# Optimization experiments

Hardware: AMD Instinct MI355X
Metric: run time of the kernel (lower is better)

Reference implementation:

```python
import jax, jax.numpy as jnp
import numpy as np

NUM_TAGS = 256
BATCH = 64
SEQ = 512


def setup_inputs() -> dict:
    key = jax.random.key(0)
    k1, k2, k3 = jax.random.split(key, 3)
    logits = jax.random.normal(k1, (BATCH, SEQ, NUM_TAGS), dtype=jnp.float32)
    tags = jax.random.randint(k2, (BATCH, SEQ), 0, NUM_TAGS, dtype=jnp.int32)
    mask = jnp.ones((BATCH, SEQ), dtype=jnp.int32)
    # learned parameter: transitions [K, K] (xavier-normal-ish init)
    std = float(np.sqrt(2.0 / (NUM_TAGS + NUM_TAGS)))
    transitions = jax.random.normal(k3, (NUM_TAGS, NUM_TAGS), dtype=jnp.float32) * std
    return {"logits": logits, "tags": tags, "mask": mask, "transitions": transitions}


def _input_likelihood(logits, mask, transitions):
    # logits: [B, S, K], mask: [B, S] float
    logits_t = jnp.transpose(logits, (1, 0, 2))  # [S, B, K]
    mask_t = jnp.transpose(mask, (1, 0))         # [S, B]
    alpha0 = logits_t[0]                          # [B, K]

    def step(alpha, xs):
        logit_i, mask_i = xs                      # [B, K], [B]
        # inner: [B, K_prev, K_next]
        inner = alpha[:, :, None] + logit_i[:, None, :] + transitions[None, :, :]
        new_alpha = jax.nn.logsumexp(inner, axis=1)
        m = mask_i[:, None]
        alpha = new_alpha * m + alpha * (1.0 - m)
        return alpha, None

    alpha, _ = jax.lax.scan(step, alpha0, (logits_t[1:], mask_t[1:]))
    return jax.nn.logsumexp(alpha, axis=-1)      # [B]


def _joint_likelihood(logits, tags, mask, transitions):
    # logits: [B, S, K], tags: [B, S] int, mask: [B, S] float
    B, S, K = logits.shape
    # transition scores for steps 0..S-2 -> transitions[tags[i], tags[i+1]] * mask[i+1]
    trans = transitions[tags[:, :-1], tags[:, 1:]] * mask[:, 1:]      # [B, S-1]
    # emit scores for steps 0..S-2 -> logits[i, tags[i]] * mask[i]
    emit = jnp.take_along_axis(logits[:, :-1], tags[:, :-1, None], axis=-1)[..., 0] * mask[:, :-1]
    score = trans.sum(axis=1) + emit.sum(axis=1)                      # [B]
    # last valid tag per batch (mask is a contiguous prefix)
    last_idx = mask.sum(axis=1).astype(jnp.int32) - 1                 # [B]
    last_tags = jnp.take_along_axis(tags, last_idx[:, None], axis=1)[:, 0]
    last_input = logits[:, -1, :][jnp.arange(B), last_tags]           # [B]
    score = score + last_input * mask[:, -1]
    return score


def reference(logits, tags, mask, transitions):
    mask_f = mask.astype(logits.dtype)
    log_num = _joint_likelihood(logits, tags, mask_f, transitions)
    log_den = _input_likelihood(logits, mask_f, transitions)
    return jnp.sum(log_num - log_den)
```

## Files before the change

### kernel.cpp

```cpp
#include <hip/hip_runtime.h>
#include <stdint.h>

#define NTAGS 256
#define BATCH 64
#define SEQ   512
#define MB    16
#define NTHREADS 256

typedef __attribute__((ext_vector_type(8))) short short8;
typedef __attribute__((ext_vector_type(4))) float f32x4;

__device__ __forceinline__ unsigned int f32_to_bf16_bits(float f) {
  unsigned int u = __float_as_uint(f);
  return (u + 0x7FFFu + ((u >> 16) & 1u)) >> 16;
}
__device__ __forceinline__ float wave_sum(float v) {
#pragma unroll
  for (int o = 32; o; o >>= 1) v += __shfl_xor(v, o);
  return v;
}
__device__ __forceinline__ unsigned int pk_bf16(float lo, float hi) {
  unsigned int r;
  asm("v_cvt_pk_bf16_f32 %0, %1, %2" : "=v"(r) : "v"(lo), "v"(hi));
  return r;
}

#define LOG2E 1.4426950408889634f

#define BAR_LGKM() \
    asm volatile("s_waitcnt lgkmcnt(0)" ::: "memory"); \
    __builtin_amdgcn_s_barrier(); \
    asm volatile("" ::: "memory");

#define MFMA_ALL(RB) \
    f32x4 acc0 = {0.f,0.f,0.f,0.f}, acc1 = {0.f,0.f,0.f,0.f}, \
          acc2 = {0.f,0.f,0.f,0.f}, acc3 = {0.f,0.f,0.f,0.f}; \
    _Pragma("unroll") \
    for (int c = 0; c < 8; ++c) { \
      const short8 bf = *(const short8*)&alds[RB][bidxs[c]]; \
      acc0 = __builtin_amdgcn_mfma_f32_16x16x32_bf16(aF[0][c], bf, acc0, 0, 0, 0); \
      acc1 = __builtin_amdgcn_mfma_f32_16x16x32_bf16(aF[1][c], bf, acc1, 0, 0, 0); \
      acc2 = __builtin_amdgcn_mfma_f32_16x16x32_bf16(aF[2][c], bf, acc2, 0, 0, 0); \
      acc3 = __builtin_amdgcn_mfma_f32_16x16x32_bf16(aF[3][c], bf, acc3, 0, 0, 0); \
    }

#define EPI_TILE_F(I, ACCI, PB, WB) { \
      const uint2 pw = PB[I]; \
      const float p0 = __uint_as_float(pw.x << 16); \
      const float p1 = __uint_as_float(pw.x & 0xFFFF0000u); \
      const float p2 = __uint_as_float(pw.y << 16); \
      const float p3 = __uint_as_float(pw.y & 0xFFFF0000u); \
      const float n0 = (MM ? ACCI[0] * p0 : sOld[I][0]) * sc; \
      const float n1 = (MM ? ACCI[1] * p1 : sOld[I][1]) * sc; \
      const float n2 = (MM ? ACCI[2] * p2 : sOld[I][2]) * sc; \
      const float n3 = (MM ? ACCI[3] * p3 : sOld[I][3]) * sc; \
      sOld[I][0] = n0; sOld[I][1] = n1; sOld[I][2] = n2; sOld[I][3] = n3; \
      mxl = fmaxf(mxl, fmaxf(fmaxf(n0, n1), fmaxf(n2, n3))); \
      uint2 wv; wv.x = pk_bf16(n0, n1); wv.y = pk_bf16(n2, n3); \
      *(uint2*)&alds[WB][widx[I]] = wv; }

#define EPI_TILE_B(I, ACCI, PB, WB) { \
      const uint2 pw = PB[I]; \
      const float p0 = __uint_as_float(pw.x << 16); \
      const float p1 = __uint_as_float(pw.x & 0xFFFF0000u); \
      const float p2 = __uint_as_float(pw.y << 16); \
      const float p3 = __uint_as_float(pw.y & 0xFFFF0000u); \
      float n0, n1, n2, n3; \
      if (fastm) { \
        n0 = ACCI[0] * p0 * sc; n1 = ACCI[1] * p1 * sc; \
        n2 = ACCI[2] * p2 * sc; n3 = ACCI[3] * p3 * sc; \
      } else { \
        const float q0 = __uint_as_float(gp[I].x << 16); \
        const float q1 = __uint_as_float(gp[I].x & 0xFFFF0000u); \
        const float q2 = __uint_as_float(gp[I].y << 16); \
        const float q3 = __uint_as_float(gp[I].y & 0xFFFF0000u); \
        n0 = (MM ? ACCI[0] * p0 : sOld[I][0] * (p0 / q0)) * sc; \
        n1 = (MM ? ACCI[1] * p1 : sOld[I][1] * (p1 / q1)) * sc; \
        n2 = (MM ? ACCI[2] * p2 : sOld[I][2] * (p2 / q2)) * sc; \
        n3 = (MM ? ACCI[3] * p3 : sOld[I][3] * (p3 / q3)) * sc; \
      } \
      gp[I] = pw; \
      sOld[I][0] = n0; sOld[I][1] = n1; sOld[I][2] = n2; sOld[I][3] = n3; \
      mxl = fmaxf(mxl, fmaxf(fmaxf(n0, n1), fmaxf(n2, n3))); \
      uint2 wv; wv.x = pk_bf16(n0, n1); wv.y = pk_bf16(n2, n3); \
      *(uint2*)&alds[WB][widx[I]] = wv; }

#define STEPF(T, RB, WB, PC, PL, MC, ML, APPLY, MEAS) { \
    { const int tp_ = ((T) + 2 < SEQ) ? ((T) + 2) : (SEQ - 1); \
      _Pragma("unroll") \
      for (int i2 = 0; i2 < 4; ++i2) PL[i2] = *(const uint2*)(Pp + tp_ * NTAGS + 16 * i2); \
      ML = mkp[tp_]; } \
    MFMA_ALL(RB) \
    float sc = 1.0f; \
    if (APPLY) { \
      const f32x4 mx4 = *(const f32x4*)&maxw[p][0]; \
      const float mx = fmaxf(fmaxf(mx4[0], mx4[1]), fmaxf(mx4[2], mx4[3])); \
      const int e = (int)((__float_as_uint(mx) >> 23) & 0xFF) - 127; \
      esum += e; \
      sc = __uint_as_float((unsigned int)(127 - e) << 23); \
    } \
    const int MM = MC; \
    float mxl = -3.0e38f; \
    EPI_TILE_F(0, acc0, PC, WB) EPI_TILE_F(1, acc1, PC, WB) \
    EPI_TILE_F(2, acc2, PC, WB) EPI_TILE_F(3, acc3, PC, WB) \
    if (MEAS) { \
      float v = mxl; v = fmaxf(v, __shfl_xor(v, 16)); v = fmaxf(v, __shfl_xor(v, 32)); \
      if (q == 0) maxw[p][wid] = v; \
    } \
    BAR_LGKM() }

#define STEPB(T, RB, WB, PC, PL, MC, ML, APPLY, MEAS) { \
    { const int tp_ = ((T) >= 2) ? ((T) - 2) : 0; \
      const int tm_ = ((T) >= 1) ? ((T) - 1) : 0; \
      _Pragma("unroll") \
      for (int i2 = 0; i2 < 4; ++i2) PL[i2] = *(const uint2*)(Pp + tp_ * NTAGS + 16 * i2); \
      ML = mkp[tm_]; } \
    MFMA_ALL(RB) \
    float sc = 1.0f; \
    if (APPLY) { \
      const f32x4 mx4 = *(const f32x4*)&maxw[p][0]; \
      const float mx = fmaxf(fmaxf(mx4[0], mx4[1]), fmaxf(mx4[2], mx4[3])); \
      const int e = (int)((__float_as_uint(mx) >> 23) & 0xFF) - 127; \
      esum += e; \
      sc = __uint_as_float((unsigned int)(127 - e) << 23); \
    } \
    const int MM = MC; \
    const bool fastm = (bool)__all(MM != 0); \
    float mxl = -3.0e38f; \
    EPI_TILE_B(0, acc0, PC, WB) EPI_TILE_B(1, acc1, PC, WB) \
    EPI_TILE_B(2, acc2, PC, WB) EPI_TILE_B(3, acc3, PC, WB) \
    if (MEAS) { \
      float v = mxl; v = fmaxf(v, __shfl_xor(v, 16)); v = fmaxf(v, __shfl_xor(v, 32)); \
      if (q == 0) maxw[p][wid] = v; \
    } \
    BAR_LGKM() }

__global__ __launch_bounds__(256)
void crf_prep(const float* __restrict__ lg, unsigned int* __restrict__ P)
{
  const size_t g = (size_t)blockIdx.x * 256 + threadIdx.x;
  const float4 a = ((const float4*)lg)[2 * g];
  const float4 b = ((const float4*)lg)[2 * g + 1];
  uint4 o;
  o.x = pk_bf16(exp2f(a.x * LOG2E), exp2f(a.y * LOG2E));
  o.y = pk_bf16(exp2f(a.z * LOG2E), exp2f(a.w * LOG2E));
  o.z = pk_bf16(exp2f(b.x * LOG2E), exp2f(b.y * LOG2E));
  o.w = pk_bf16(exp2f(b.z * LOG2E), exp2f(b.w * LOG2E));
  ((uint4*)P)[g] = o;
}

__global__ __launch_bounds__(NTHREADS, 1)
void crf_halves(const unsigned short* __restrict__ P,
                const int*   __restrict__ mask,
                const float* __restrict__ trans,
                float* __restrict__ wsA, float* __restrict__ wsB,
                int* __restrict__ wseF, int* __restrict__ wseB)
{
  const int bid  = blockIdx.x;
  const int bwd  = bid >> 2;
  const int b0   = (bid & 3) * MB;
  const int tid  = threadIdx.x;
  const int wid  = tid >> 6;
  const int lane = tid & 63;
  const int p    = lane & 15;
  const int q    = lane >> 4;

  __shared__ __align__(16) short alds[2][NTAGS * MB];
  __shared__ __align__(16) float maxw[16][4];

  const unsigned short* Pp = P + (size_t)(b0 + p) * SEQ * NTAGS + 64 * wid + 4 * q;
  const int* mkp = mask + (b0 + p) * SEQ;

  int bidxs[8], widx[4];
#pragma unroll
  for (int c = 0; c < 8; ++c) bidxs[c] = (p * NTAGS + 32 * c + 8 * q) ^ ((p & 7) << 3);
#pragma unroll
  for (int i = 0; i < 4; ++i) widx[i] = (p * NTAGS + 64 * wid + 16 * i + 4 * q) ^ ((p & 7) << 3);

  short8 aF[4][8];
#pragma unroll
  for (int i = 0; i < 4; ++i) {
    const int m = 64 * wid + 16 * i + p;
#pragma unroll
    for (int c = 0; c < 8; ++c) {
      short8 w;
#pragma unroll
      for (int j = 0; j < 8; ++j) {
        const int tag = 32 * c + 8 * q + j;
        const float tv = bwd ? trans[m * NTAGS + tag] : trans[tag * NTAGS + m];
        w[j] = (short)f32_to_bf16_bits(exp2f(tv * LOG2E));
      }
      aF[i][c] = w;
    }
  }

  f32x4 sOld[4];
  uint2 p0[4], p1[4], p2[4], p3[4], gp[4];
  int m0 = 1, m1 = 1, m2 = 1, m3 = 1;
  int esum = 0;

  if (!bwd) {
#pragma unroll
    for (int i = 0; i < 4; ++i) {
      const uint2 pw = *(const uint2*)(Pp + 16 * i);
      f32x4 a;
      a[0] = __uint_as_float(pw.x << 16); a[1] = __uint_as_float(pw.x & 0xFFFF0000u);
      a[2] = __uint_as_float(pw.y << 16); a[3] = __uint_as_float(pw.y & 0xFFFF0000u);
      sOld[i] = a;
      *(uint2*)&alds[0][widx[i]] = pw;
    }
#pragma unroll
    for (int i = 0; i < 4; ++i) {
      p1[i] = *(const uint2*)(Pp + 1 * NTAGS + 16 * i);
      p2[i] = *(const uint2*)(Pp + 2 * NTAGS + 16 * i);
    }
    m1 = mkp[1]; m2 = mkp[2];
    __syncthreads();

    STEPF(1, 0, 1, p1, p3, m1, m3, 0, 0)
    STEPF(2, 1, 0, p2, p0, m2, m0, 0, 0)
    STEPF(3, 0, 1, p3, p1, m3, m1, 0, 1)
#pragma unroll 1
    for (int tb = 4; tb <= 248; tb += 4) {
      STEPF(tb + 0, 1, 0, p0, p2, m0, m2, 1, 0)
      STEPF(tb + 1, 0, 1, p1, p3, m1, m3, 0, 0)
      STEPF(tb + 2, 1, 0, p2, p0, m2, m0, 0, 0)
      STEPF(tb + 3, 0, 1, p3, p1, m3, m1, 0, 1)
    }
    STEPF(252, 1, 0, p0, p2, m0, m2, 1, 0)
    STEPF(253, 0, 1, p1, p3, m1, m3, 0, 0)
    STEPF(254, 1, 0, p2, p0, m2, m0, 0, 0)

    {
      MFMA_ALL(0)
      const int MM = m3;
      float* wp = wsA + (size_t)(b0 + p) * NTAGS + 64 * wid + 4 * q;
#pragma unroll
      for (int i = 0; i < 4; ++i) {
        const uint2 pw = p3[i];
        f32x4 pv;
        pv[0] = __uint_as_float(pw.x << 16); pv[1] = __uint_as_float(pw.x & 0xFFFF0000u);
        pv[2] = __uint_as_float(pw.y << 16); pv[3] = __uint_as_float(pw.y & 0xFFFF0000u);
        f32x4 o;
        const f32x4 ac = (i == 0) ? acc0 : (i == 1) ? acc1 : (i == 2) ? acc2 : acc3;
#pragma unroll
        for (int r = 0; r < 4; ++r)
          o[r] = MM ? ac[r] * pv[r] : sOld[i][r];
        *(f32x4*)(wp + 16 * i) = o;
      }
    }
    if (tid < 16) wseF[b0 + tid] = esum;
  } else {
#pragma unroll
    for (int i = 0; i < 4; ++i) {
      const uint2 pw = *(const uint2*)(Pp + (SEQ - 1) * NTAGS + 16 * i);
      f32x4 a;
      a[0] = __uint_as_float(pw.x << 16); a[1] = __uint_as_float(pw.x & 0xFFFF0000u);
      a[2] = __uint_as_float(pw.y << 16); a[3] = __uint_as_float(pw.y & 0xFFFF0000u);
      sOld[i] = a; gp[i] = pw;
      *(uint2*)&alds[0][widx[i]] = pw;
    }
#pragma unroll
    for (int i = 0; i < 4; ++i) {
      p2[i] = *(const uint2*)(Pp + 510 * NTAGS + 16 * i);
      p1[i] = *(const uint2*)(Pp + 509 * NTAGS + 16 * i);
    }
    m2 = mkp[511];
    m1 = mkp[510];
    __syncthreads();

    STEPB(510, 0, 1, p2, p0, m2, m0, 0, 0)
    STEPB(509, 1, 0, p1, p3, m1, m3, 0, 0)
    STEPB(508, 0, 1, p0, p2, m0, m2, 0, 1)
#pragma unroll 1
    for (int tb = 507; tb >= 263; tb -= 4) {
      STEPB(tb - 0, 1, 0, p3, p1, m3, m1, 1, 0)
      STEPB(tb - 1, 0, 1, p2, p0, m2, m0, 0, 0)
      STEPB(tb - 2, 1, 0, p1, p3, m1, m3, 0, 0)
      STEPB(tb - 3, 0, 1, p0, p2, m0, m2, 0, 1)
    }
    STEPB(259, 1, 0, p3, p1, m3, m1, 1, 0)
    STEPB(258, 0, 1, p2, p0, m2, m0, 0, 0)
    STEPB(257, 1, 0, p1, p3, m1, m3, 0, 0)
    STEPB(256, 0, 1, p0, p2, m0, m2, 0, 0)

    {
      MFMA_ALL(1)
      float* wp = wsB + (size_t)(b0 + p) * NTAGS + 64 * wid + 4 * q;
      *(f32x4*)(wp + 0)  = acc0;
      *(f32x4*)(wp + 16) = acc1;
      *(f32x4*)(wp + 32) = acc2;
      *(f32x4*)(wp + 48) = acc3;
    }
    if (tid < 16) wseB[b0 + tid] = esum;
  }
}

__global__ __launch_bounds__(256)
void crf_combine(const float* __restrict__ logits,
                 const int*   __restrict__ tags,
                 const int*   __restrict__ mask,
                 const float* __restrict__ trans,
                 const float* __restrict__ wsA,
                 const float* __restrict__ wsB,
                 const int*   __restrict__ wseF,
                 const int*   __restrict__ wseB,
                 float* __restrict__ out)
{
  const int b    = blockIdx.x;
  const int tid  = threadIdx.x;
  const int lane = tid & 63;
  const int wid  = tid >> 6;

  __shared__ float rn[4], rm[4], rp[4];

  const float LN2 = 0.6931471805599453f;
  const float* lg = logits + (size_t)b * SEQ * NTAGS;
  const int*   tg = tags + b * SEQ;
  const int*   mk = mask + b * SEQ;

  float numer = 0.f, msum = 0.f;
  for (int t = tid; t < SEQ; t += 256) {
    int   tag_t = tg[t];
    float m_t   = (float)mk[t];
    msum += m_t;
    if (t < SEQ - 1) {
      numer += lg[t * NTAGS + tag_t] * m_t;
      numer += trans[tag_t * NTAGS + tg[t + 1]] * (float)mk[t + 1];
    }
  }
  numer = wave_sum(numer);
  msum  = wave_sum(msum);
  if (lane == 0) { rn[wid] = numer; rm[wid] = msum; }

  float pprod = wsA[b * NTAGS + tid] * wsB[b * NTAGS + tid];
  pprod = wave_sum(pprod);
  if (lane == 0) rp[wid] = pprod;
  __syncthreads();

  if (tid == 0) {
    const float numer_tot = (rn[0] + rn[1]) + (rn[2] + rn[3]);
    const float msum_tot  = (rm[0] + rm[1]) + (rm[2] + rm[3]);
    const float psum      = (rp[0] + rp[1]) + (rp[2] + rp[3]);
    const float log_den   = logf(psum) + (float)(wseF[b] + wseB[b]) * LN2;
    int last_idx = (int)msum_tot - 1;
    if (last_idx < 0) last_idx = 0;
    const int last_tag = tg[last_idx];
    const float score = numer_tot + lg[(SEQ - 1) * NTAGS + last_tag] * (float)mk[SEQ - 1];
    atomicAdd(out, score - log_den);
  }
}

extern "C" void kernel_launch(void* const* d_in, const int* in_sizes, int n_in,
                              void* d_out, int out_size, void* d_ws, size_t ws_size,
                              hipStream_t stream) {
  const float* logits = (const float*)d_in[0];
  const int*   tags   = (const int*)d_in[1];
  const int*   mask   = (const int*)d_in[2];
  const float* trans  = (const float*)d_in[3];
  float* out = (float*)d_out;

  unsigned short* P = (unsigned short*)d_ws;
  float* wsA  = (float*)((char*)d_ws + (size_t)BATCH * SEQ * NTAGS * 2);
  float* wsB  = wsA + BATCH * NTAGS;
  int*   wseF = (int*)(wsB + BATCH * NTAGS);
  int*   wseB = wseF + BATCH;

  hipMemsetAsync(out, 0, sizeof(float), stream);
  crf_prep<<<dim3(BATCH * SEQ * NTAGS / (256 * 8)), dim3(256), 0, stream>>>(logits, (unsigned int*)P);
  crf_halves<<<dim3(8), dim3(NTHREADS), 0, stream>>>(P, mask, trans, wsA, wsB, wseF, wseB);
  crf_combine<<<dim3(BATCH), dim3(256), 0, stream>>>(logits, tags, mask, trans, wsA, wsB, wseF, wseB, out);
}
```

Baseline: 286.0 us.

## Merge forward and backward chains into one 512-thread block per batch group

```diff
diff --git a/kernel.cpp b/kernel.cpp
--- a/kernel.cpp
+++ b/kernel.cpp
@@ -5,7 +5,7 @@
 #define BATCH 64
 #define SEQ   512
 #define MB    16
-#define NTHREADS 256
+#define NTHREADS 512
 
 typedef __attribute__((ext_vector_type(8))) short short8;
 typedef __attribute__((ext_vector_type(4))) float f32x4;
@@ -37,88 +37,56 @@
           acc2 = {0.f,0.f,0.f,0.f}, acc3 = {0.f,0.f,0.f,0.f}; \
     _Pragma("unroll") \
     for (int c = 0; c < 8; ++c) { \
-      const short8 bf = *(const short8*)&alds[RB][bidxs[c]]; \
+      const short8 bf = *(const short8*)&aldsC[RB][bidxs[c]]; \
       acc0 = __builtin_amdgcn_mfma_f32_16x16x32_bf16(aF[0][c], bf, acc0, 0, 0, 0); \
       acc1 = __builtin_amdgcn_mfma_f32_16x16x32_bf16(aF[1][c], bf, acc1, 0, 0, 0); \
       acc2 = __builtin_amdgcn_mfma_f32_16x16x32_bf16(aF[2][c], bf, acc2, 0, 0, 0); \
       acc3 = __builtin_amdgcn_mfma_f32_16x16x32_bf16(aF[3][c], bf, acc3, 0, 0, 0); \
     }
 
-#define EPI_TILE_F(I, ACCI, PB, WB) { \
+#define EPI_TILE(I, ACCI, PB, WB, ME) { \
       const uint2 pw = PB[I]; \
-      const float p0 = __uint_as_float(pw.x << 16); \
-      const float p1 = __uint_as_float(pw.x & 0xFFFF0000u); \
-      const float p2 = __uint_as_float(pw.y << 16); \
-      const float p3 = __uint_as_float(pw.y & 0xFFFF0000u); \
-      const float n0 = (MM ? ACCI[0] * p0 : sOld[I][0]) * sc; \
-      const float n1 = (MM ? ACCI[1] * p1 : sOld[I][1]) * sc; \
-      const float n2 = (MM ? ACCI[2] * p2 : sOld[I][2]) * sc; \
-      const float n3 = (MM ? ACCI[3] * p3 : sOld[I][3]) * sc; \
-      sOld[I][0] = n0; sOld[I][1] = n1; sOld[I][2] = n2; sOld[I][3] = n3; \
-      mxl = fmaxf(mxl, fmaxf(fmaxf(n0, n1), fmaxf(n2, n3))); \
-      uint2 wv; wv.x = pk_bf16(n0, n1); wv.y = pk_bf16(n2, n3); \
-      *(uint2*)&alds[WB][widx[I]] = wv; }
-
-#define EPI_TILE_B(I, ACCI, PB, WB) { \
-      const uint2 pw = PB[I]; \
-      const float p0 = __uint_as_float(pw.x << 16); \
-      const float p1 = __uint_as_float(pw.x & 0xFFFF0000u); \
-      const float p2 = __uint_as_float(pw.y << 16); \
-      const float p3 = __uint_as_float(pw.y & 0xFFFF0000u); \
+      const float p0_ = __uint_as_float(pw.x << 16); \
+      const float p1_ = __uint_as_float(pw.x & 0xFFFF0000u); \
+      const float p2_ = __uint_as_float(pw.y << 16); \
+      const float p3_ = __uint_as_float(pw.y & 0xFFFF0000u); \
       float n0, n1, n2, n3; \
       if (fastm) { \
-        n0 = ACCI[0] * p0 * sc; n1 = ACCI[1] * p1 * sc; \
-        n2 = ACCI[2] * p2 * sc; n3 = ACCI[3] * p3 * sc; \
+        n0 = ACCI[0] * p0_ * sc; n1 = ACCI[1] * p1_ * sc; \
+        n2 = ACCI[2] * p2_ * sc; n3 = ACCI[3] * p3_ * sc; \
+      } else if (!chain) { \
+        n0 = (MM ? ACCI[0] * p0_ : sOld[I][0]) * sc; \
+        n1 = (MM ? ACCI[1] * p1_ : sOld[I][1]) * sc; \
+        n2 = (MM ? ACCI[2] * p2_ : sOld[I][2]) * sc; \
+        n3 = (MM ? ACCI[3] * p3_ : sOld[I][3]) * sc; \
       } else { \
-        const float q0 = __uint_as_float(gp[I].x << 16); \
-        const float q1 = __uint_as_float(gp[I].x & 0xFFFF0000u); \
-        const float q2 = __uint_as_float(gp[I].y << 16); \
-        const float q3 = __uint_as_float(gp[I].y & 0xFFFF0000u); \
-        n0 = (MM ? ACCI[0] * p0 : sOld[I][0] * (p0 / q0)) * sc; \
-        n1 = (MM ? ACCI[1] * p1 : sOld[I][1] * (p1 / q1)) * sc; \
-        n2 = (MM ? ACCI[2] * p2 : sOld[I][2] * (p2 / q2)) * sc; \
-        n3 = (MM ? ACCI[3] * p3 : sOld[I][3] * (p3 / q3)) * sc; \
+        const float q0_ = __uint_as_float(gp[I].x << 16); \
+        const float q1_ = __uint_as_float(gp[I].x & 0xFFFF0000u); \
+        const float q2_ = __uint_as_float(gp[I].y << 16); \
+        const float q3_ = __uint_as_float(gp[I].y & 0xFFFF0000u); \
+        n0 = (MM ? ACCI[0] * p0_ : sOld[I][0] * (p0_ / q0_)) * sc; \
+        n1 = (MM ? ACCI[1] * p1_ : sOld[I][1] * (p1_ / q1_)) * sc; \
+        n2 = (MM ? ACCI[2] * p2_ : sOld[I][2] * (p2_ / q2_)) * sc; \
+        n3 = (MM ? ACCI[3] * p3_ : sOld[I][3] * (p3_ / q3_)) * sc; \
       } \
       gp[I] = pw; \
       sOld[I][0] = n0; sOld[I][1] = n1; sOld[I][2] = n2; sOld[I][3] = n3; \
-      mxl = fmaxf(mxl, fmaxf(fmaxf(n0, n1), fmaxf(n2, n3))); \
+      if (ME) mxl = fmaxf(mxl, fmaxf(fmaxf(n0, n1), fmaxf(n2, n3))); \
       uint2 wv; wv.x = pk_bf16(n0, n1); wv.y = pk_bf16(n2, n3); \
-      *(uint2*)&alds[WB][widx[I]] = wv; }
-
-#define STEPF(T, RB, WB, PC, PL, MC, ML, APPLY, MEAS) { \
-    { const int tp_ = ((T) + 2 < SEQ) ? ((T) + 2) : (SEQ - 1); \
+      *(uint2*)&aldsC[WB][widx[I]] = wv; }
+
+#define STEP(S, RB, WB, PC, PL, MC, ML, APPLY, MEAS) { \
+    { int tpP_ = chain ? 509 - (S) : (S) + 2; \
+      int tpM_ = chain ? 510 - (S) : (S) + 2; \
+      tpP_ = tpP_ < 0 ? 0 : (tpP_ > SEQ - 1 ? SEQ - 1 : tpP_); \
+      tpM_ = tpM_ < 0 ? 0 : (tpM_ > SEQ - 1 ? SEQ - 1 : tpM_); \
       _Pragma("unroll") \
-      for (int i2 = 0; i2 < 4; ++i2) PL[i2] = *(const uint2*)(Pp + tp_ * NTAGS + 16 * i2); \
-      ML = mkp[tp_]; } \
+      for (int i2 = 0; i2 < 4; ++i2) PL[i2] = *(const uint2*)(Pp + (size_t)tpP_ * NTAGS + 16 * i2); \
+      ML = mkp[tpM_]; } \
     MFMA_ALL(RB) \
     float sc = 1.0f; \
     if (APPLY) { \
-      const f32x4 mx4 = *(const f32x4*)&maxw[p][0]; \
-      const float mx = fmaxf(fmaxf(mx4[0], mx4[1]), fmaxf(mx4[2], mx4[3])); \
-      const int e = (int)((__float_as_uint(mx) >> 23) & 0xFF) - 127; \
-      esum += e; \
-      sc = __uint_as_float((unsigned int)(127 - e) << 23); \
-    } \
-    const int MM = MC; \
-    float mxl = -3.0e38f; \
-    EPI_TILE_F(0, acc0, PC, WB) EPI_TILE_F(1, acc1, PC, WB) \
-    EPI_TILE_F(2, acc2, PC, WB) EPI_TILE_F(3, acc3, PC, WB) \
-    if (MEAS) { \
-      float v = mxl; v = fmaxf(v, __shfl_xor(v, 16)); v = fmaxf(v, __shfl_xor(v, 32)); \
-      if (q == 0) maxw[p][wid] = v; \
-    } \
-    BAR_LGKM() }
-
-#define STEPB(T, RB, WB, PC, PL, MC, ML, APPLY, MEAS) { \
-    { const int tp_ = ((T) >= 2) ? ((T) - 2) : 0; \
-      const int tm_ = ((T) >= 1) ? ((T) - 1) : 0; \
-      _Pragma("unroll") \
-      for (int i2 = 0; i2 < 4; ++i2) PL[i2] = *(const uint2*)(Pp + tp_ * NTAGS + 16 * i2); \
-      ML = mkp[tm_]; } \
-    MFMA_ALL(RB) \
-    float sc = 1.0f; \
-    if (APPLY) { \
-      const f32x4 mx4 = *(const f32x4*)&maxw[p][0]; \
+      const f32x4 mx4 = *(const f32x4*)&maxwC[p][0]; \
       const float mx = fmaxf(fmaxf(mx4[0], mx4[1]), fmaxf(mx4[2], mx4[3])); \
       const int e = (int)((__float_as_uint(mx) >> 23) & 0xFF) - 127; \
       esum += e; \
@@ -127,11 +95,11 @@
     const int MM = MC; \
     const bool fastm = (bool)__all(MM != 0); \
     float mxl = -3.0e38f; \
-    EPI_TILE_B(0, acc0, PC, WB) EPI_TILE_B(1, acc1, PC, WB) \
-    EPI_TILE_B(2, acc2, PC, WB) EPI_TILE_B(3, acc3, PC, WB) \
+    EPI_TILE(0, acc0, PC, WB, MEAS) EPI_TILE(1, acc1, PC, WB, MEAS) \
+    EPI_TILE(2, acc2, PC, WB, MEAS) EPI_TILE(3, acc3, PC, WB, MEAS) \
     if (MEAS) { \
       float v = mxl; v = fmaxf(v, __shfl_xor(v, 16)); v = fmaxf(v, __shfl_xor(v, 32)); \
-      if (q == 0) maxw[p][wid] = v; \
+      if (q == 0) maxwC[p][cw] = v; \
     } \
     BAR_LGKM() }
 
@@ -156,38 +124,42 @@
                 float* __restrict__ wsA, float* __restrict__ wsB,
                 int* __restrict__ wseF, int* __restrict__ wseB)
 {
-  const int bid  = blockIdx.x;
-  const int bwd  = bid >> 2;
-  const int b0   = (bid & 3) * MB;
-  const int tid  = threadIdx.x;
-  const int wid  = tid >> 6;
-  const int lane = tid & 63;
-  const int p    = lane & 15;
-  const int q    = lane >> 4;
-
-  __shared__ __align__(16) short alds[2][NTAGS * MB];
-  __shared__ __align__(16) float maxw[16][4];
-
-  const unsigned short* Pp = P + (size_t)(b0 + p) * SEQ * NTAGS + 64 * wid + 4 * q;
+  const int bid   = blockIdx.x;
+  const int b0    = bid * MB;
+  const int tid   = threadIdx.x;
+  const int wid   = tid >> 6;
+  const int chain = wid >> 2;
+  const int cw    = wid & 3;
+  const int lane  = tid & 63;
+  const int p     = lane & 15;
+  const int q     = lane >> 4;
+
+  __shared__ __align__(16) short alds[2][2][NTAGS * MB];
+  __shared__ __align__(16) float maxw[2][16][4];
+
+  short (*aldsC)[NTAGS * MB] = alds[chain];
+  float (*maxwC)[4]          = maxw[chain];
+
+  const unsigned short* Pp = P + (size_t)(b0 + p) * SEQ * NTAGS + 64 * cw + 4 * q;
   const int* mkp = mask + (b0 + p) * SEQ;
 
   int bidxs[8], widx[4];
 #pragma unroll
   for (int c = 0; c < 8; ++c) bidxs[c] = (p * NTAGS + 32 * c + 8 * q) ^ ((p & 7) << 3);
 #pragma unroll
-  for (int i = 0; i < 4; ++i) widx[i] = (p * NTAGS + 64 * wid + 16 * i + 4 * q) ^ ((p & 7) << 3);
+  for (int i = 0; i < 4; ++i) widx[i] = (p * NTAGS + 64 * cw + 16 * i + 4 * q) ^ ((p & 7) << 3);
 
   short8 aF[4][8];
 #pragma unroll
   for (int i = 0; i < 4; ++i) {
-    const int m = 64 * wid + 16 * i + p;
+    const int m = 64 * cw + 16 * i + p;
 #pragma unroll
     for (int c = 0; c < 8; ++c) {
       short8 w;
 #pragma unroll
       for (int j = 0; j < 8; ++j) {
         const int tag = 32 * c + 8 * q + j;
-        const float tv = bwd ? trans[m * NTAGS + tag] : trans[tag * NTAGS + m];
+        const float tv = chain ? trans[m * NTAGS + tag] : trans[tag * NTAGS + m];
         w[j] = (short)f32_to_bf16_bits(exp2f(tv * LOG2E));
       }
       aF[i][c] = w;
@@ -199,42 +171,49 @@
   int m0 = 1, m1 = 1, m2 = 1, m3 = 1;
   int esum = 0;
 
-  if (!bwd) {
+  {
+    const int t0  = chain ? (SEQ - 1) : 0;
+    const int t1P = chain ? 510 : 1;
+    const int t1M = chain ? 511 : 1;
+    const int t2P = chain ? 509 : 2;
+    const int t2M = chain ? 510 : 2;
 #pragma unroll
     for (int i = 0; i < 4; ++i) {
-      const uint2 pw = *(const uint2*)(Pp + 16 * i);
+      const uint2 pw = *(const uint2*)(Pp + (size_t)t0 * NTAGS + 16 * i);
       f32x4 a;
       a[0] = __uint_as_float(pw.x << 16); a[1] = __uint_as_float(pw.x & 0xFFFF0000u);
       a[2] = __uint_as_float(pw.y << 16); a[3] = __uint_as_float(pw.y & 0xFFFF0000u);
-      sOld[i] = a;
-      *(uint2*)&alds[0][widx[i]] = pw;
+      sOld[i] = a; gp[i] = pw;
+      *(uint2*)&aldsC[0][widx[i]] = pw;
     }
 #pragma unroll
     for (int i = 0; i < 4; ++i) {
-      p1[i] = *(const uint2*)(Pp + 1 * NTAGS + 16 * i);
-      p2[i] = *(const uint2*)(Pp + 2 * NTAGS + 16 * i);
-    }
-    m1 = mkp[1]; m2 = mkp[2];
-    __syncthreads();
-
-    STEPF(1, 0, 1, p1, p3, m1, m3, 0, 0)
-    STEPF(2, 1, 0, p2, p0, m2, m0, 0, 0)
-    STEPF(3, 0, 1, p3, p1, m3, m1, 0, 1)
+      p1[i] = *(const uint2*)(Pp + (size_t)t1P * NTAGS + 16 * i);
+      p2[i] = *(const uint2*)(Pp + (size_t)t2P * NTAGS + 16 * i);
+    }
+    m1 = mkp[t1M]; m2 = mkp[t2M];
+  }
+  __syncthreads();
+
+  STEP(1, 0, 1, p1, p3, m1, m3, 0, 0)
+  STEP(2, 1, 0, p2, p0, m2, m0, 0, 0)
+  STEP(3, 0, 1, p3, p1, m3, m1, 0, 1)
 #pragma unroll 1
-    for (int tb = 4; tb <= 248; tb += 4) {
-      STEPF(tb + 0, 1, 0, p0, p2, m0, m2, 1, 0)
-      STEPF(tb + 1, 0, 1, p1, p3, m1, m3, 0, 0)
-      STEPF(tb + 2, 1, 0, p2, p0, m2, m0, 0, 0)
-      STEPF(tb + 3, 0, 1, p3, p1, m3, m1, 0, 1)
-    }
-    STEPF(252, 1, 0, p0, p2, m0, m2, 1, 0)
-    STEPF(253, 0, 1, p1, p3, m1, m3, 0, 0)
-    STEPF(254, 1, 0, p2, p0, m2, m0, 0, 0)
-
-    {
-      MFMA_ALL(0)
+  for (int s0 = 4; s0 <= 248; s0 += 4) {
+    STEP(s0 + 0, 1, 0, p0, p2, m0, m2, 1, 0)
+    STEP(s0 + 1, 0, 1, p1, p3, m1, m3, 0, 0)
+    STEP(s0 + 2, 1, 0, p2, p0, m2, m0, 0, 0)
+    STEP(s0 + 3, 0, 1, p3, p1, m3, m1, 0, 1)
+  }
+  STEP(252, 1, 0, p0, p2, m0, m2, 1, 0)
+  STEP(253, 0, 1, p1, p3, m1, m3, 0, 0)
+  STEP(254, 1, 0, p2, p0, m2, m0, 0, 0)
+
+  {
+    MFMA_ALL(0)
+    if (!chain) {
       const int MM = m3;
-      float* wp = wsA + (size_t)(b0 + p) * NTAGS + 64 * wid + 4 * q;
+      float* wp = wsA + (size_t)(b0 + p) * NTAGS + 64 * cw + 4 * q;
 #pragma unroll
       for (int i = 0; i < 4; ++i) {
         const uint2 pw = p3[i];
@@ -248,51 +227,27 @@
           o[r] = MM ? ac[r] * pv[r] : sOld[i][r];
         *(f32x4*)(wp + 16 * i) = o;
       }
-    }
-    if (tid < 16) wseF[b0 + tid] = esum;
-  } else {
-#pragma unroll
-    for (int i = 0; i < 4; ++i) {
-      const uint2 pw = *(const uint2*)(Pp + (SEQ - 1) * NTAGS + 16 * i);
-      f32x4 a;
-      a[0] = __uint_as_float(pw.x << 16); a[1] = __uint_as_float(pw.x & 0xFFFF0000u);
-      a[2] = __uint_as_float(pw.y << 16); a[3] = __uint_as_float(pw.y & 0xFFFF0000u);
-      sOld[i] = a; gp[i] = pw;
-      *(uint2*)&alds[0][widx[i]] = pw;
-    }
-#pragma unroll
-    for (int i = 0; i < 4; ++i) {
-      p2[i] = *(const uint2*)(Pp + 510 * NTAGS + 16 * i);
-      p1[i] = *(const uint2*)(Pp + 509 * NTAGS + 16 * i);
-    }
-    m2 = mkp[511];
-    m1 = mkp[510];
-    __syncthreads();
-
-    STEPB(510, 0, 1, p2, p0, m2, m0, 0, 0)
-    STEPB(509, 1, 0, p1, p3, m1, m3, 0, 0)
-    STEPB(508, 0, 1, p0, p2, m0, m2, 0, 1)
-#pragma unroll 1
-    for (int tb = 507; tb >= 263; tb -= 4) {
-      STEPB(tb - 0, 1, 0, p3, p1, m3, m1, 1, 0)
-      STEPB(tb - 1, 0, 1, p2, p0, m2, m0, 0, 0)
-      STEPB(tb - 2, 1, 0, p1, p3, m1, m3, 0, 0)
-      STEPB(tb - 3, 0, 1, p0, p2, m0, m2, 0, 1)
-    }
-    STEPB(259, 1, 0, p3, p1, m3, m1, 1, 0)
-    STEPB(258, 0, 1, p2, p0, m2, m0, 0, 0)
-    STEPB(257, 1, 0, p1, p3, m1, m3, 0, 0)
-    STEPB(256, 0, 1, p0, p2, m0, m2, 0, 0)
-
-    {
-      MFMA_ALL(1)
-      float* wp = wsB + (size_t)(b0 + p) * NTAGS + 64 * wid + 4 * q;
-      *(f32x4*)(wp + 0)  = acc0;
-      *(f32x4*)(wp + 16) = acc1;
-      *(f32x4*)(wp + 32) = acc2;
-      *(f32x4*)(wp + 48) = acc3;
-    }
-    if (tid < 16) wseB[b0 + tid] = esum;
+      if (wid == 0 && lane < 16) wseF[b0 + lane] = esum;
+    } else {
+      const float sc = 1.0f;
+      const int MM = m3;
+      const bool fastm = (bool)__all(MM != 0);
+      float mxl = -3.0e38f;
+      EPI_TILE(0, acc0, p3, 1, 0) EPI_TILE(1, acc1, p3, 1, 0)
+      EPI_TILE(2, acc2, p3, 1, 0) EPI_TILE(3, acc3, p3, 1, 0)
+      (void)mxl;
+    }
+  }
+  BAR_LGKM()
+
+  if (chain) {
+    MFMA_ALL(1)
+    float* wp = wsB + (size_t)(b0 + p) * NTAGS + 64 * cw + 4 * q;
+    *(f32x4*)(wp + 0)  = acc0;
+    *(f32x4*)(wp + 16) = acc1;
+    *(f32x4*)(wp + 32) = acc2;
+    *(f32x4*)(wp + 48) = acc3;
+    if (cw == 0 && lane < 16) wseB[b0 + lane] = esum;
   }
 }
 
@@ -368,6 +323,6 @@
 
   hipMemsetAsync(out, 0, sizeof(float), stream);
   crf_prep<<<dim3(BATCH * SEQ * NTAGS / (256 * 8)), dim3(256), 0, stream>>>(logits, (unsigned int*)P);
-  crf_halves<<<dim3(8), dim3(NTHREADS), 0, stream>>>(P, mask, trans, wsA, wsB, wseF, wseB);
+  crf_halves<<<dim3(4), dim3(NTHREADS), 0, stream>>>(P, mask, trans, wsA, wsB, wseF, wseB);
   crf_combine<<<dim3(BATCH), dim3(256), 0, stream>>>(logits, tags, mask, trans, wsA, wsB, wseF, wseB, out);
 }
```

Result: slower. 439.0 us (+53.5%).

## Split CRF recurrence across eight waves per block instead of four

Applied to the files above, without the earlier changes.

```diff
diff --git a/kernel.cpp b/kernel.cpp
--- a/kernel.cpp
+++ b/kernel.cpp
@@ -5,7 +5,7 @@
 #define BATCH 64
 #define SEQ   512
 #define MB    16
-#define NTHREADS 256
+#define NTHREADS 512
 
 typedef __attribute__((ext_vector_type(8))) short short8;
 typedef __attribute__((ext_vector_type(4))) float f32x4;
@@ -33,76 +33,75 @@
     asm volatile("" ::: "memory");
 
 #define MFMA_ALL(RB) \
-    f32x4 acc0 = {0.f,0.f,0.f,0.f}, acc1 = {0.f,0.f,0.f,0.f}, \
-          acc2 = {0.f,0.f,0.f,0.f}, acc3 = {0.f,0.f,0.f,0.f}; \
+    f32x4 acc0 = {0.f,0.f,0.f,0.f}, acc1 = {0.f,0.f,0.f,0.f}; \
     _Pragma("unroll") \
     for (int c = 0; c < 8; ++c) { \
       const short8 bf = *(const short8*)&alds[RB][bidxs[c]]; \
       acc0 = __builtin_amdgcn_mfma_f32_16x16x32_bf16(aF[0][c], bf, acc0, 0, 0, 0); \
       acc1 = __builtin_amdgcn_mfma_f32_16x16x32_bf16(aF[1][c], bf, acc1, 0, 0, 0); \
-      acc2 = __builtin_amdgcn_mfma_f32_16x16x32_bf16(aF[2][c], bf, acc2, 0, 0, 0); \
-      acc3 = __builtin_amdgcn_mfma_f32_16x16x32_bf16(aF[3][c], bf, acc3, 0, 0, 0); \
-    }
-
-#define EPI_TILE_F(I, ACCI, PB, WB) { \
+    }
+
+#define EPI_TILE_F(I, ACCI, PB, WB, ME) { \
       const uint2 pw = PB[I]; \
-      const float p0 = __uint_as_float(pw.x << 16); \
-      const float p1 = __uint_as_float(pw.x & 0xFFFF0000u); \
-      const float p2 = __uint_as_float(pw.y << 16); \
-      const float p3 = __uint_as_float(pw.y & 0xFFFF0000u); \
-      const float n0 = (MM ? ACCI[0] * p0 : sOld[I][0]) * sc; \
-      const float n1 = (MM ? ACCI[1] * p1 : sOld[I][1]) * sc; \
-      const float n2 = (MM ? ACCI[2] * p2 : sOld[I][2]) * sc; \
-      const float n3 = (MM ? ACCI[3] * p3 : sOld[I][3]) * sc; \
+      const float p0_ = __uint_as_float(pw.x << 16); \
+      const float p1_ = __uint_as_float(pw.x & 0xFFFF0000u); \
+      const float p2_ = __uint_as_float(pw.y << 16); \
+      const float p3_ = __uint_as_float(pw.y & 0xFFFF0000u); \
+      const float n0 = (MM ? ACCI[0] * p0_ : sOld[I][0]) * sc; \
+      const float n1 = (MM ? ACCI[1] * p1_ : sOld[I][1]) * sc; \
+      const float n2 = (MM ? ACCI[2] * p2_ : sOld[I][2]) * sc; \
+      const float n3 = (MM ? ACCI[3] * p3_ : sOld[I][3]) * sc; \
       sOld[I][0] = n0; sOld[I][1] = n1; sOld[I][2] = n2; sOld[I][3] = n3; \
-      mxl = fmaxf(mxl, fmaxf(fmaxf(n0, n1), fmaxf(n2, n3))); \
+      if (ME) mxl = fmaxf(mxl, fmaxf(fmaxf(n0, n1), fmaxf(n2, n3))); \
       uint2 wv; wv.x = pk_bf16(n0, n1); wv.y = pk_bf16(n2, n3); \
       *(uint2*)&alds[WB][widx[I]] = wv; }
 
-#define EPI_TILE_B(I, ACCI, PB, WB) { \
+#define EPI_TILE_B(I, ACCI, PB, WB, ME) { \
       const uint2 pw = PB[I]; \
-      const float p0 = __uint_as_float(pw.x << 16); \
-      const float p1 = __uint_as_float(pw.x & 0xFFFF0000u); \
-      const float p2 = __uint_as_float(pw.y << 16); \
-      const float p3 = __uint_as_float(pw.y & 0xFFFF0000u); \
+      const float p0_ = __uint_as_float(pw.x << 16); \
+      const float p1_ = __uint_as_float(pw.x & 0xFFFF0000u); \
+      const float p2_ = __uint_as_float(pw.y << 16); \
+      const float p3_ = __uint_as_float(pw.y & 0xFFFF0000u); \
       float n0, n1, n2, n3; \
       if (fastm) { \
-        n0 = ACCI[0] * p0 * sc; n1 = ACCI[1] * p1 * sc; \
-        n2 = ACCI[2] * p2 * sc; n3 = ACCI[3] * p3 * sc; \
+        n0 = ACCI[0] * p0_ * sc; n1 = ACCI[1] * p1_ * sc; \
+        n2 = ACCI[2] * p2_ * sc; n3 = ACCI[3] * p3_ * sc; \
       } else { \
-        const float q0 = __uint_as_float(gp[I].x << 16); \
-        const float q1 = __uint_as_float(gp[I].x & 0xFFFF0000u); \
-        const float q2 = __uint_as_float(gp[I].y << 16); \
-        const float q3 = __uint_as_float(gp[I].y & 0xFFFF0000u); \
-        n0 = (MM ? ACCI[0] * p0 : sOld[I][0] * (p0 / q0)) * sc; \
-        n1 = (MM ? ACCI[1] * p1 : sOld[I][1] * (p1 / q1)) * sc; \
-        n2 = (MM ? ACCI[2] * p2 : sOld[I][2] * (p2 / q2)) * sc; \
-        n3 = (MM ? ACCI[3] * p3 : sOld[I][3] * (p3 / q3)) * sc; \
+        const float q0_ = __uint_as_float(gp[I].x << 16); \
+        const float q1_ = __uint_as_float(gp[I].x & 0xFFFF0000u); \
+        const float q2_ = __uint_as_float(gp[I].y << 16); \
+        const float q3_ = __uint_as_float(gp[I].y & 0xFFFF0000u); \
+        n0 = (MM ? ACCI[0] * p0_ : sOld[I][0] * (p0_ / q0_)) * sc; \
+        n1 = (MM ? ACCI[1] * p1_ : sOld[I][1] * (p1_ / q1_)) * sc; \
+        n2 = (MM ? ACCI[2] * p2_ : sOld[I][2] * (p2_ / q2_)) * sc; \
+        n3 = (MM ? ACCI[3] * p3_ : sOld[I][3] * (p3_ / q3_)) * sc; \
       } \
       gp[I] = pw; \
       sOld[I][0] = n0; sOld[I][1] = n1; sOld[I][2] = n2; sOld[I][3] = n3; \
-      mxl = fmaxf(mxl, fmaxf(fmaxf(n0, n1), fmaxf(n2, n3))); \
+      if (ME) mxl = fmaxf(mxl, fmaxf(fmaxf(n0, n1), fmaxf(n2, n3))); \
       uint2 wv; wv.x = pk_bf16(n0, n1); wv.y = pk_bf16(n2, n3); \
       *(uint2*)&alds[WB][widx[I]] = wv; }
+
+#define APPLY_BODY() { \
+      const f32x4 mxa = *(const f32x4*)&maxw[p][0]; \
+      const f32x4 mxb = *(const f32x4*)&maxw[p][4]; \
+      const float mx = fmaxf(fmaxf(fmaxf(mxa[0], mxa[1]), fmaxf(mxa[2], mxa[3])), \
+                             fmaxf(fmaxf(mxb[0], mxb[1]), fmaxf(mxb[2], mxb[3]))); \
+      const int e = (int)((__float_as_uint(mx) >> 23) & 0xFF) - 127; \
+      esum += e; \
+      sc = __uint_as_float((unsigned int)(127 - e) << 23); }
 
 #define STEPF(T, RB, WB, PC, PL, MC, ML, APPLY, MEAS) { \
     { const int tp_ = ((T) + 2 < SEQ) ? ((T) + 2) : (SEQ - 1); \
       _Pragma("unroll") \
-      for (int i2 = 0; i2 < 4; ++i2) PL[i2] = *(const uint2*)(Pp + tp_ * NTAGS + 16 * i2); \
+      for (int i2 = 0; i2 < 2; ++i2) PL[i2] = *(const uint2*)(Pp + (size_t)tp_ * NTAGS + 16 * i2); \
       ML = mkp[tp_]; } \
     MFMA_ALL(RB) \
     float sc = 1.0f; \
-    if (APPLY) { \
-      const f32x4 mx4 = *(const f32x4*)&maxw[p][0]; \
-      const float mx = fmaxf(fmaxf(mx4[0], mx4[1]), fmaxf(mx4[2], mx4[3])); \
-      const int e = (int)((__float_as_uint(mx) >> 23) & 0xFF) - 127; \
-      esum += e; \
-      sc = __uint_as_float((unsigned int)(127 - e) << 23); \
-    } \
+    if (APPLY) APPLY_BODY() \
     const int MM = MC; \
     float mxl = -3.0e38f; \
-    EPI_TILE_F(0, acc0, PC, WB) EPI_TILE_F(1, acc1, PC, WB) \
-    EPI_TILE_F(2, acc2, PC, WB) EPI_TILE_F(3, acc3, PC, WB) \
+    EPI_TILE_F(0, acc0, PC, WB, MEAS) EPI_TILE_F(1, acc1, PC, WB, MEAS) \
     if (MEAS) { \
       float v = mxl; v = fmaxf(v, __shfl_xor(v, 16)); v = fmaxf(v, __shfl_xor(v, 32)); \
       if (q == 0) maxw[p][wid] = v; \
@@ -113,22 +112,15 @@
     { const int tp_ = ((T) >= 2) ? ((T) - 2) : 0; \
       const int tm_ = ((T) >= 1) ? ((T) - 1) : 0; \
       _Pragma("unroll") \
-      for (int i2 = 0; i2 < 4; ++i2) PL[i2] = *(const uint2*)(Pp + tp_ * NTAGS + 16 * i2); \
+      for (int i2 = 0; i2 < 2; ++i2) PL[i2] = *(const uint2*)(Pp + (size_t)tp_ * NTAGS + 16 * i2); \
       ML = mkp[tm_]; } \
     MFMA_ALL(RB) \
     float sc = 1.0f; \
-    if (APPLY) { \
-      const f32x4 mx4 = *(const f32x4*)&maxw[p][0]; \
-      const float mx = fmaxf(fmaxf(mx4[0], mx4[1]), fmaxf(mx4[2], mx4[3])); \
-      const int e = (int)((__float_as_uint(mx) >> 23) & 0xFF) - 127; \
-      esum += e; \
-      sc = __uint_as_float((unsigned int)(127 - e) << 23); \
-    } \
+    if (APPLY) APPLY_BODY() \
     const int MM = MC; \
     const bool fastm = (bool)__all(MM != 0); \
     float mxl = -3.0e38f; \
-    EPI_TILE_B(0, acc0, PC, WB) EPI_TILE_B(1, acc1, PC, WB) \
-    EPI_TILE_B(2, acc2, PC, WB) EPI_TILE_B(3, acc3, PC, WB) \
+    EPI_TILE_B(0, acc0, PC, WB, MEAS) EPI_TILE_B(1, acc1, PC, WB, MEAS) \
     if (MEAS) { \
       float v = mxl; v = fmaxf(v, __shfl_xor(v, 16)); v = fmaxf(v, __shfl_xor(v, 32)); \
       if (q == 0) maxw[p][wid] = v; \
@@ -149,7 +141,7 @@
   ((uint4*)P)[g] = o;
 }
 
-__global__ __launch_bounds__(NTHREADS, 1)
+__global__ __launch_bounds__(NTHREADS, 2)
 void crf_halves(const unsigned short* __restrict__ P,
                 const int*   __restrict__ mask,
                 const float* __restrict__ trans,
@@ -166,21 +158,21 @@
   const int q    = lane >> 4;
 
   __shared__ __align__(16) short alds[2][NTAGS * MB];
-  __shared__ __align__(16) float maxw[16][4];
-
-  const unsigned short* Pp = P + (size_t)(b0 + p) * SEQ * NTAGS + 64 * wid + 4 * q;
+  __shared__ __align__(32) float maxw[16][8];
+
+  const unsigned short* Pp = P + (size_t)(b0 + p) * SEQ * NTAGS + 32 * wid + 4 * q;
   const int* mkp = mask + (b0 + p) * SEQ;
 
-  int bidxs[8], widx[4];
+  int bidxs[8], widx[2];
 #pragma unroll
   for (int c = 0; c < 8; ++c) bidxs[c] = (p * NTAGS + 32 * c + 8 * q) ^ ((p & 7) << 3);
 #pragma unroll
-  for (int i = 0; i < 4; ++i) widx[i] = (p * NTAGS + 64 * wid + 16 * i + 4 * q) ^ ((p & 7) << 3);
-
-  short8 aF[4][8];
-#pragma unroll
-  for (int i = 0; i < 4; ++i) {
-    const int m = 64 * wid + 16 * i + p;
+  for (int i = 0; i < 2; ++i) widx[i] = (p * NTAGS + 32 * wid + 16 * i + 4 * q) ^ ((p & 7) << 3);
+
+  short8 aF[2][8];
+#pragma unroll
+  for (int i = 0; i < 2; ++i) {
+    const int m = 32 * wid + 16 * i + p;
 #pragma unroll
     for (int c = 0; c < 8; ++c) {
       short8 w;
@@ -194,14 +186,14 @@
     }
   }
 
-  f32x4 sOld[4];
-  uint2 p0[4], p1[4], p2[4], p3[4], gp[4];
+  f32x4 sOld[2];
+  uint2 p0[2], p1[2], p2[2], p3[2], gp[2];
   int m0 = 1, m1 = 1, m2 = 1, m3 = 1;
   int esum = 0;
 
   if (!bwd) {
 #pragma unroll
-    for (int i = 0; i < 4; ++i) {
+    for (int i = 0; i < 2; ++i) {
       const uint2 pw = *(const uint2*)(Pp + 16 * i);
       f32x4 a;
       a[0] = __uint_as_float(pw.x << 16); a[1] = __uint_as_float(pw.x & 0xFFFF0000u);
@@ -210,7 +202,7 @@
       *(uint2*)&alds[0][widx[i]] = pw;
     }
 #pragma unroll
-    for (int i = 0; i < 4; ++i) {
+    for (int i = 0; i < 2; ++i) {
       p1[i] = *(const uint2*)(Pp + 1 * NTAGS + 16 * i);
       p2[i] = *(const uint2*)(Pp + 2 * NTAGS + 16 * i);
     }
@@ -234,15 +226,15 @@
     {
       MFMA_ALL(0)
       const int MM = m3;
-      float* wp = wsA + (size_t)(b0 + p) * NTAGS + 64 * wid + 4 * q;
-#pragma unroll
-      for (int i = 0; i < 4; ++i) {
+      float* wp = wsA + (size_t)(b0 + p) * NTAGS + 32 * wid + 4 * q;
+#pragma unroll
+      for (int i = 0; i < 2; ++i) {
         const uint2 pw = p3[i];
         f32x4 pv;
         pv[0] = __uint_as_float(pw.x << 16); pv[1] = __uint_as_float(pw.x & 0xFFFF0000u);
         pv[2] = __uint_as_float(pw.y << 16); pv[3] = __uint_as_float(pw.y & 0xFFFF0000u);
         f32x4 o;
-        const f32x4 ac = (i == 0) ? acc0 : (i == 1) ? acc1 : (i == 2) ? acc2 : acc3;
+        const f32x4 ac = (i == 0) ? acc0 : acc1;
 #pragma unroll
         for (int r = 0; r < 4; ++r)
           o[r] = MM ? ac[r] * pv[r] : sOld[i][r];
@@ -252,8 +244,8 @@
     if (tid < 16) wseF[b0 + tid] = esum;
   } else {
 #pragma unroll
-    for (int i = 0; i < 4; ++i) {
-      const uint2 pw = *(const uint2*)(Pp + (SEQ - 1) * NTAGS + 16 * i);
+    for (int i = 0; i < 2; ++i) {
+      const uint2 pw = *(const uint2*)(Pp + (size_t)(SEQ - 1) * NTAGS + 16 * i);
       f32x4 a;
       a[0] = __uint_as_float(pw.x << 16); a[1] = __uint_as_float(pw.x & 0xFFFF0000u);
       a[2] = __uint_as_float(pw.y << 16); a[3] = __uint_as_float(pw.y & 0xFFFF0000u);
@@ -261,9 +253,9 @@
       *(uint2*)&alds[0][widx[i]] = pw;
     }
 #pragma unroll
-    for (int i = 0; i < 4; ++i) {
-      p2[i] = *(const uint2*)(Pp + 510 * NTAGS + 16 * i);
-      p1[i] = *(const uint2*)(Pp + 509 * NTAGS + 16 * i);
+    for (int i = 0; i < 2; ++i) {
+      p2[i] = *(const uint2*)(Pp + (size_t)510 * NTAGS + 16 * i);
+      p1[i] = *(const uint2*)(Pp + (size_t)509 * NTAGS + 16 * i);
     }
     m2 = mkp[511];
     m1 = mkp[510];
@@ -286,11 +278,9 @@
 
     {
       MFMA_ALL(1)
-      float* wp = wsB + (size_t)(b0 + p) * NTAGS + 64 * wid + 4 * q;
+      float* wp = wsB + (size_t)(b0 + p) * NTAGS + 32 * wid + 4 * q;
       *(f32x4*)(wp + 0)  = acc0;
       *(f32x4*)(wp + 16) = acc1;
-      *(f32x4*)(wp + 32) = acc2;
-      *(f32x4*)(wp + 48) = acc3;
     }
     if (tid < 16) wseB[b0 + tid] = esum;
   }
```

Result: faster. 280.1 us (-2.1%).
